# Performance work log

Measured on AMD Instinct MI355X. Metric: run time of the kernel, lower is better.

The kernel has to match this reference:

```python
import jax, jax.numpy as jnp
import numpy as np

B, L, W, MODES, NL, SEG, CM, H1 = 8, 8192, 128, 32, 4, 4, 8, 128


def gelu(x):
    return jax.nn.gelu(x, approximate=False)  # torch nn.GELU default = exact erf


def cft(h, w):
    # h: [b, c, l]; w: [SEG, CM, c_in, c_out] (Chebyshev weights for one layer)
    b, c, l = h.shape
    ls = l // SEG
    xs = h.reshape(b, c, SEG, ls)
    # per-segment global min/max normalization (over batch, channel, position)
    mn = xs.min(axis=(0, 1, 3), keepdims=True)
    mx = xs.max(axis=(0, 1, 3), keepdims=True)
    xn = 2.0 * (xs - mn) / (mx - mn) - 1.0
    Tpp = jnp.ones_like(xn)
    Tp = xn
    coeffs = [(xn * Tpp).mean(-1), (xn * Tp).mean(-1)]  # each [b, c, SEG]
    for _ in range(2, CM):
        Tn = 2.0 * xn * Tp - Tpp
        coeffs.append((xn * Tn).mean(-1))
        Tpp, Tp = Tp, Tn
    C = jnp.stack(coeffs[:CM], axis=-1)  # [b, c, SEG, CM]
    filt = jnp.einsum('bcsm,smco->bcso', C, w)  # per-segment mode filtering
    rec = jnp.tanh(filt.mean(-1))  # [b, c, SEG]
    return jnp.broadcast_to(rec[..., None], (b, c, SEG, ls)).reshape(b, c, l)


def setup_inputs() -> dict:
    key = jax.random.key(0)
    ks = jax.random.split(key, 12)
    scale = 1.0 / (W * W)
    p = {}
    p['x'] = jax.random.normal(ks[0], (B, L, 2), jnp.float32)
    p['fc0_w'] = jax.random.normal(ks[1], (2, W), jnp.float32) * 0.1
    p['fc0_b'] = jnp.zeros((W,), jnp.float32)
    p['spec_wr'] = jax.random.uniform(ks[2], (NL, W, W, MODES), jnp.float32) * scale
    p['spec_wi'] = jax.random.uniform(ks[3], (NL, W, W, MODES), jnp.float32) * scale
    p['conv_w'] = jax.random.normal(ks[4], (NL, W, W), jnp.float32) * 0.05
    p['conv_b'] = jnp.zeros((NL, W), jnp.float32)
    p['cheb_w'] = jax.random.normal(ks[5], (NL, SEG, CM, W, W), jnp.float32) * 0.02
    p['gate_w'] = jax.random.normal(ks[6], (NL, 2 * W, W), jnp.float32) * 0.05
    p['gate_b'] = jnp.zeros((NL, W), jnp.float32)
    p['fc1_w'] = jax.random.normal(ks[7], (W, H1), jnp.float32) * 0.05
    p['fc1_b'] = jnp.zeros((H1,), jnp.float32)
    p['fc2_w'] = jax.random.normal(ks[8], (H1, 1), jnp.float32) * 0.05
    p['fc2_b'] = jnp.zeros((1,), jnp.float32)
    return p


def reference(x, fc0_w, fc0_b, spec_wr, spec_wi, conv_w, conv_b, cheb_w,
              gate_w, gate_b, fc1_w, fc1_b, fc2_w, fc2_b):
    nfreq = L // 2 + 1
    h = x @ fc0_w + fc0_b          # [B, L, W]
    h = h.transpose(0, 2, 1)       # [B, W, L]
    for i in range(NL):
        # --- spectral conv ---
        hf = jnp.fft.rfft(h)       # [B, W, nfreq] complex64
        wgt = spec_wr[i] + 1j * spec_wi[i]
        om = jnp.einsum('bix,iox->box', hf[:, :, :MODES], wgt)
        out_ft = jnp.pad(om, ((0, 0), (0, 0), (0, nfreq - MODES)))
        sp = jnp.fft.irfft(out_ft, n=L)
        # --- 1x1 conv bypass ---
        pw = jnp.einsum('io,bil->bol', conv_w[i], h) + conv_b[i][None, :, None]
        x_fno = gelu(sp + pw)
        # --- CFT branch ---
        x_cft = cft(h, cheb_w[i])
        # --- gated fusion ---
        cat = jnp.concatenate([x_fno, x_cft], axis=1).transpose(0, 2, 1)  # [B, L, 2W]
        gate = jax.nn.sigmoid(cat @ gate_w[i] + gate_b[i]).transpose(0, 2, 1)
        h = x_fno + gate * x_cft
    h = h.transpose(0, 2, 1)       # [B, L, W]
    h = gelu(h @ fc1_w + fc1_b)
    return h @ fc2_w + fc2_b       # [B, L, 1]
```

## Files before the change

### kernel.cpp

```cpp
#include <hip/hip_runtime.h>
#include <math.h>


#define OFF_COSTAB 0
#define OFF_SINTAB 8192
#define OFF_BASTC  16384
#define OFF_BASTS  (OFF_BASTC + 262144)
#define OFF_UNUSED (OFF_BASTS + 262144)
#define OFF_WBAR   (OFF_UNUSED + 65536)
#define OFF_HFP    (OFF_WBAR + 16384)
#define OFF_HF     (OFF_HFP + 1048576)
#define OFF_CH     (OFF_HF + 65536)
#define OFF_REC    (OFF_CH + 32768)
#define OFF_OMCT   (OFF_REC + 4096)
#define OFF_OMST   (OFF_OMCT + 32768)
#define OFF_CG     (OFF_OMST + 32768)
#define OFF_MNMX   (OFF_CG + 4096)
#define OFF_H      (OFF_MNMX + 16)

__device__ __forceinline__ unsigned int enc_f(float f) {
    unsigned int u = __float_as_uint(f);
    return (u & 0x80000000u) ? ~u : (u | 0x80000000u);
}
__device__ __forceinline__ float dec_f(unsigned int u) {
    return (u & 0x80000000u) ? __uint_as_float(u ^ 0x80000000u) : __uint_as_float(~u);
}
__device__ __forceinline__ float gelu_f(float x) {
    return 0.5f * x * (1.0f + erff(x * 0.70710678118654752f));
}
__device__ __forceinline__ float sigmoid_f(float x) {
    return 1.0f / (1.0f + expf(-x));
}

constexpr float C32T[32] = {
    1.0f,          0.980785280f,  0.923879533f,  0.831469612f,
    0.707106781f,  0.555570233f,  0.382683432f,  0.195090322f,
    0.0f,         -0.195090322f, -0.382683432f, -0.555570233f,
   -0.707106781f, -0.831469612f, -0.923879533f, -0.980785280f,
   -1.0f,         -0.980785280f, -0.923879533f, -0.831469612f,
   -0.707106781f, -0.555570233f, -0.382683432f, -0.195090322f,
    0.0f,          0.195090322f,  0.382683432f,  0.555570233f,
    0.707106781f,  0.831469612f,  0.923879533f,  0.980785280f};
constexpr float S32T[32] = {
    0.0f,          0.195090322f,  0.382683432f,  0.555570233f,
    0.707106781f,  0.831469612f,  0.923879533f,  0.980785280f,
    1.0f,          0.980785280f,  0.923879533f,  0.831469612f,
    0.707106781f,  0.555570233f,  0.382683432f,  0.195090322f,
    0.0f,         -0.195090322f, -0.382683432f, -0.555570233f,
   -0.707106781f, -0.831469612f, -0.923879533f, -0.980785280f,
   -1.0f,         -0.980785280f, -0.923879533f, -0.831469612f,
   -0.707106781f, -0.555570233f, -0.382683432f, -0.195090322f};

__global__ void k_tab(float* ws) {
    int m = blockIdx.x * 256 + threadIdx.x;
    if (m < 8192) {
        double a = (double)m * (6.283185307179586476925286766559 / 8192.0);
        ws[OFF_COSTAB + m] = (float)cos(a);
        ws[OFF_SINTAB + m] = (float)sin(a);
    }
}

__global__ void k_init2(float* ws, const float* __restrict__ cheb_w) {
    int tid = blockIdx.x * 256 + threadIdx.x;
    if (tid < 524288) {
        int j = tid >> 13, l = tid & 8191;
        int k = j & 31;
        int tab = (j < 32) ? OFF_COSTAB : OFF_SINTAB;
        ws[OFF_BASTC + tid] = ws[tab + ((k * l) & 8191)];
    } else if (tid < 524288 + 16384) {
        int r = tid - 524288;
        int c = r & 127;
        int smi = r >> 7;
        const float* wp = cheb_w + ((long)smi * 128 + c) * 128;
        float s = 0.0f;
        for (int o = 0; o < 128; o++) s += wp[o];
        ws[OFF_WBAR + r] = s * (1.0f / 128.0f);
    } else if (tid < 524288 + 16384 + 8) {
        int r = tid - (524288 + 16384);
        unsigned int* mm = (unsigned int*)(ws + OFF_MNMX);
        mm[r] = (r < 4) ? 0xFFFFFFFFu : 0u;
    }
}

__global__ __launch_bounds__(256) void k_fc0(float* ws, const float* __restrict__ x,
                                             const float* __restrict__ w,
                                             const float* __restrict__ bias) {
    int bid = blockIdx.x;
    int b = bid >> 5;
    int l0 = (bid & 31) * 256;
    int t = threadIdx.x;
    int l = l0 + t;
    float x0 = x[((long)b * 8192 + l) * 2];
    float x1 = x[((long)b * 8192 + l) * 2 + 1];
    float* hb = ws + OFF_H + (long)b * 128 * 8192;
    float mn = 1e30f, mx = -1e30f;
    for (int c = 0; c < 128; c++) {
        float v = fmaf(x0, w[c], fmaf(x1, w[128 + c], bias[c]));
        hb[(long)c * 8192 + l] = v;
        mn = fminf(mn, v); mx = fmaxf(mx, v);
    }
    for (int off = 32; off; off >>= 1) {
        mn = fminf(mn, __shfl_down(mn, off));
        mx = fmaxf(mx, __shfl_down(mx, off));
    }
    __shared__ float rmn[4], rmx[4];
    if ((t & 63) == 0) { rmn[t >> 6] = mn; rmx[t >> 6] = mx; }
    __syncthreads();
    if (t == 0) {
        for (int w2 = 1; w2 < 4; w2++) { mn = fminf(mn, rmn[w2]); mx = fmaxf(mx, rmx[w2]); }
        unsigned int* mm = (unsigned int*)(ws + OFF_MNMX);
        int seg = l0 >> 11;
        atomicMin(&mm[seg], enc_f(mn));
        atomicMax(&mm[4 + seg], enc_f(mx));
    }
}

__global__ __launch_bounds__(256, 4) void k_dftcb(float* ws, int layer) {
    int row = blockIdx.x;
    int t = threadIdx.x;
    const float* hr = ws + OFF_H + (long)row * 8192;
    __shared__ float red[4][96];
    int wv = t >> 6;

    float ha[32];
    #pragma unroll
    for (int a = 0; a < 32; a++) ha[a] = hr[a * 256 + t];

    const unsigned int* mm = (const unsigned int*)(ws + OFF_MNMX);
    #pragma unroll
    for (int s = 0; s < 4; s++) {
        float mn = dec_f(mm[s]), mx = dec_f(mm[4 + s]);
        float sc = 2.0f / (mx - mn);
        float acc[8] = {};
        #pragma unroll
        for (int e = 0; e < 8; e++) {
            float xn = (ha[s * 8 + e] - mn) * sc - 1.0f;
            float tpp = 1.0f, tp = xn;
            acc[0] += xn;
            acc[1] += xn * xn;
            #pragma unroll
            for (int mI = 2; mI < 8; mI++) {
                float tn = 2.0f * xn * tp - tpp;
                acc[mI] += xn * tn;
                tpp = tp; tp = tn;
            }
        }
        #pragma unroll
        for (int mI = 0; mI < 8; mI++) {
            float v = acc[mI];
            for (int off = 32; off; off >>= 1) v += __shfl_down(v, off);
            if ((t & 63) == 0) red[wv][64 + s * 8 + mI] = v;
        }
    }

    float ep[16], em[16];
    #pragma unroll
    for (int a = 1; a < 16; a++) { ep[a] = ha[a] + ha[32 - a]; em[a] = ha[a] - ha[32 - a]; }
    float h0 = ha[0], h16 = ha[16];
    float Ca[17], Sa[17];
    #pragma unroll
    for (int k = 0; k <= 16; k++) {
        float ca = (k & 1) ? (h0 - h16) : (h0 + h16);
        float sa = 0.0f;
        #pragma unroll
        for (int a = 1; a < 16; a++) {
            ca = fmaf(ep[a], C32T[(k * a) & 31], ca);
            sa = fmaf(em[a], S32T[(k * a) & 31], sa);
        }
        Ca[k] = ca; Sa[k] = sa;
    }

    const float* ct = ws + OFF_COSTAB;
    const float* st = ws + OFF_SINTAB;
    #pragma unroll
    for (int k0 = 0; k0 < 32; k0 += 8) {
        float xr[8], xi[8];
        #pragma unroll
        for (int q = 0; q < 8; q++) {
            int k = k0 + q;
            float caf = (k <= 16) ? Ca[k] : Ca[32 - k];
            float saf = (k <= 16) ? Sa[k] : -Sa[32 - k];
            float c = ct[(k * t) & 8191];
            float s = st[(k * t) & 8191];
            xr[q] = caf * c - saf * s;
            xi[q] = fmaf(saf, c, caf * s);
        }
        #pragma unroll
        for (int q = 0; q < 8; q++) {
            float a = xr[q], b2 = xi[q];
            for (int off = 32; off; off >>= 1) {
                a += __shfl_down(a, off);
                b2 += __shfl_down(b2, off);
            }
            if ((t & 63) == 0) { red[wv][k0 + q] = a; red[wv][32 + k0 + q] = b2; }
        }
    }
    __syncthreads();
    if (t < 96) {
        float s4 = red[0][t] + red[1][t] + red[2][t] + red[3][t];
        if (t < 64) {
            ws[OFF_HF + (long)row * 64 + t] = s4;
        } else {
            red[0][t] = s4 * (1.0f / 2048.0f);
        }
    }
    __syncthreads();
    if (t < 4) {
        const float* wb = ws + OFF_WBAR + ((layer * 4 + t) * 8) * 128 + (row & 127);
        float a = 0.0f;
        #pragma unroll
        for (int mI = 0; mI < 8; mI++) a = fmaf(red[0][64 + t * 8 + mI], wb[mI * 128], a);
        ws[OFF_REC + (long)row * 4 + t] = tanhf(a);
    }
}

__global__ void k_b2(float* ws, const float* __restrict__ swr, const float* __restrict__ swi,
                     const float* __restrict__ gw, const float* __restrict__ gb, int layer) {
    int tid = blockIdx.x * 256 + threadIdx.x;
    if (tid < 32768) {
        int b = tid >> 12, o = (tid >> 5) & 127, k = tid & 31;
        const float* hfb = ws + OFF_HF + (long)b * 8192;
        const float* wr = swr + (long)layer * 524288 + (long)o * 32 + k;
        const float* wi = swi + (long)layer * 524288 + (long)o * 32 + k;
        float omr = 0.0f, omi = 0.0f;
        for (int i = 0; i < 128; i++) {
            float hr = hfb[i * 64 + k];
            float hs = hfb[i * 64 + 32 + k];
            float wrv = wr[(long)i * 4096], wiv = wi[(long)i * 4096];
            omr = fmaf(hr, wrv, fmaf(hs, wiv, omr));
            omi = fmaf(hr, wiv, fmaf(-hs, wrv, omi));
        }
        float ck = (k == 0) ? (1.0f / 8192.0f) : (2.0f / 8192.0f);
        ws[OFF_OMCT + ((long)b * 32 + k) * 128 + o] = ck * omr;
        ws[OFF_OMST + ((long)b * 32 + k) * 128 + o] = -ck * omi;
    } else if (tid < 32768 + 4096) {
        int r = tid - 32768;
        int b = r >> 9, s = (r >> 7) & 3, o = r & 127;
        float a = gb[layer * 128 + o];
        const float* recp = ws + OFF_REC + (long)b * 512 + s;
        const float* g2 = gw + (long)layer * 32768 + 16384 + o;
        for (int c = 0; c < 128; c++) a = fmaf(recp[c * 4], g2[c * 128], a);
        ws[OFF_CG + (long)(b * 4 + s) * 128 + o] = a;
    }
    if (blockIdx.x == gridDim.x - 1 && threadIdx.x < 8) {
        unsigned int* mm = (unsigned int*)(ws + OFF_MNMX);
        mm[threadIdx.x] = (threadIdx.x < 4) ? 0xFFFFFFFFu : 0u;
    }
}

__global__ __launch_bounds__(512, 4) void k_fuse(
    float* __restrict__ hglob,
    const float* __restrict__ basc,
    const float* __restrict__ bass,
    const float* __restrict__ omct,
    const float* __restrict__ omst,
    const float* __restrict__ rec,
    const float* __restrict__ cgt,
    unsigned int* __restrict__ mnmx,
    const float* __restrict__ cw, const float* __restrict__ cb,
    const float* __restrict__ gw, int layer) {
    __shared__ float hx[128 * 128];
    __shared__ float rmn[8], rmx[8];
    int bid = blockIdx.x;
    int b = bid >> 6;
    int l0 = (bid & 63) * 128;
    int seg = l0 >> 11;
    int t = threadIdx.x;
    float* hb = hglob + (long)b * 1048576;

    #pragma unroll
    for (int i = 0; i < 8; i++) {
        int idx = t + i * 512;
        int row = idx >> 5, c4 = (idx & 31) * 4;
        *(float4*)&hx[row * 128 + c4] = *(const float4*)&hb[(long)row * 8192 + l0 + c4];
    }
    __syncthreads();

    int p = t & 63;
    int c0 = __builtin_amdgcn_readfirstlane((t >> 6) * 16);

    float acc0[16] = {}, acc1[16] = {};

    const float* btp = basc + l0 + p;
    const float* bsp = bass + l0 + p;
    const float* omc = omct + (long)b * 4096 + c0;
    const float* oms = omst + (long)b * 4096 + c0;
    #pragma unroll 2
    for (int k = 0; k < 32; k++) {
        float bc0 = btp[k * 8192];
        float bc1 = btp[k * 8192 + 64];
        float bs0 = bsp[k * 8192];
        float bs1 = bsp[k * 8192 + 64];
        #pragma unroll
        for (int c = 0; c < 16; c++) {
            float wc = omc[k * 128 + c], wsn = oms[k * 128 + c];
            acc0[c] = fmaf(wc, bc0, fmaf(wsn, bs0, acc0[c]));
            acc1[c] = fmaf(wc, bc1, fmaf(wsn, bs1, acc1[c]));
        }
    }
    const float* cwt = cw + (long)layer * 16384 + c0;
    #pragma unroll 2
    for (int j = 0; j < 128; j++) {
        float hv0 = hx[j * 128 + p];
        float hv1 = hx[j * 128 + 64 + p];
        #pragma unroll
        for (int c = 0; c < 16; c++) {
            float wv = cwt[j * 128 + c];
            acc0[c] = fmaf(wv, hv0, acc0[c]);
            acc1[c] = fmaf(wv, hv1, acc1[c]);
        }
    }
    const float* cbl = cb + layer * 128 + c0;
    #pragma unroll
    for (int c = 0; c < 16; c++) {
        acc0[c] = gelu_f(acc0[c] + cbl[c]);
        acc1[c] = gelu_f(acc1[c] + cbl[c]);
    }
    __syncthreads();
    #pragma unroll
    for (int c = 0; c < 16; c++) {
        hx[(c0 + c) * 128 + p] = acc0[c];
        hx[(c0 + c) * 128 + 64 + p] = acc1[c];
    }
    __syncthreads();

    const float* gwl = gw + (long)layer * 32768 + c0;
    float gac0[16] = {}, gac1[16] = {};
    #pragma unroll 2
    for (int j = 0; j < 128; j++) {
        float xv0 = hx[j * 128 + p];
        float xv1 = hx[j * 128 + 64 + p];
        #pragma unroll
        for (int c = 0; c < 16; c++) {
            float wv = gwl[j * 128 + c];
            gac0[c] = fmaf(wv, xv0, gac0[c]);
            gac1[c] = fmaf(wv, xv1, gac1[c]);
        }
    }
    const float* cgp = cgt + (long)(b * 4 + seg) * 128 + c0;
    const float* rcp = rec + (long)(b * 128 + c0) * 4 + seg;
    float mnv = 1e30f, mxv = -1e30f;
    #pragma unroll
    for (int c = 0; c < 16; c++) {
        float cgv = cgp[c];
        float rv = rcp[c * 4];
        float g0 = sigmoid_f(gac0[c] + cgv);
        float g1 = sigmoid_f(gac1[c] + cgv);
        float v0 = fmaf(g0, rv, acc0[c]);
        float v1 = fmaf(g1, rv, acc1[c]);
        mnv = fminf(mnv, fminf(v0, v1));
        mxv = fmaxf(mxv, fmaxf(v0, v1));
        hb[(long)(c0 + c) * 8192 + l0 + p] = v0;
        hb[(long)(c0 + c) * 8192 + l0 + 64 + p] = v1;
    }
    for (int off = 32; off; off >>= 1) {
        mnv = fminf(mnv, __shfl_down(mnv, off));
        mxv = fmaxf(mxv, __shfl_down(mxv, off));
    }
    if ((t & 63) == 0) { rmn[t >> 6] = mnv; rmx[t >> 6] = mxv; }
    __syncthreads();
    if (t == 0) {
        for (int w2 = 1; w2 < 8; w2++) { mnv = fminf(mnv, rmn[w2]); mxv = fmaxf(mxv, rmx[w2]); }
        atomicMin(&mnmx[seg], enc_f(mnv));
        atomicMax(&mnmx[4 + seg], enc_f(mxv));
    }
}

__global__ __launch_bounds__(512, 4) void k_fc12(
    const float* __restrict__ hglob, const float* __restrict__ f1w,
    const float* __restrict__ f1b, const float* __restrict__ f2w,
    const float* __restrict__ f2b, float* __restrict__ out) {
    __shared__ float hx[128 * 128];
    int bid = blockIdx.x;
    int b = bid >> 6;
    int l0 = (bid & 63) * 128;
    int t = threadIdx.x;
    const float* hb = hglob + (long)b * 1048576;
    #pragma unroll
    for (int i = 0; i < 8; i++) {
        int idx = t + i * 512;
        int row = idx >> 5, c4 = (idx & 31) * 4;
        *(float4*)&hx[row * 128 + c4] = *(const float4*)&hb[(long)row * 8192 + l0 + c4];
    }
    __syncthreads();
    int p = t & 63;
    int h0 = __builtin_amdgcn_readfirstlane((t >> 6) * 16);
    float acc0[16] = {}, acc1[16] = {};
    const float* f1 = f1w + h0;
    #pragma unroll 2
    for (int j = 0; j < 128; j++) {
        float xv0 = hx[j * 128 + p];
        float xv1 = hx[j * 128 + 64 + p];
        #pragma unroll
        for (int c = 0; c < 16; c++) {
            float wv = f1[j * 128 + c];
            acc0[c] = fmaf(wv, xv0, acc0[c]);
            acc1[c] = fmaf(wv, xv1, acc1[c]);
        }
    }
    float outp0 = 0.0f, outp1 = 0.0f;
    #pragma unroll
    for (int c = 0; c < 16; c++) {
        float bias = f1b[h0 + c];
        float fw = f2w[h0 + c];
        outp0 = fmaf(fw, gelu_f(acc0[c] + bias), outp0);
        outp1 = fmaf(fw, gelu_f(acc1[c] + bias), outp1);
    }
    __syncthreads();
    hx[(t >> 6) * 128 + p] = outp0;
    hx[(t >> 6) * 128 + 64 + p] = outp1;
    __syncthreads();
    if (t < 128) {
        float s = f2b[0];
        #pragma unroll
        for (int gg = 0; gg < 8; gg++) s += hx[gg * 128 + t];
        out[(long)b * 8192 + l0 + t] = s;
    }
}

extern "C" void kernel_launch(void* const* d_in, const int* in_sizes, int n_in,
                              void* d_out, int out_size, void* d_ws, size_t ws_size,
                              hipStream_t stream) {
    const float* x     = (const float*)d_in[0];
    const float* fc0_w = (const float*)d_in[1];
    const float* fc0_b = (const float*)d_in[2];
    const float* swr   = (const float*)d_in[3];
    const float* swi   = (const float*)d_in[4];
    const float* cw    = (const float*)d_in[5];
    const float* cb    = (const float*)d_in[6];
    const float* chw   = (const float*)d_in[7];
    const float* gw    = (const float*)d_in[8];
    const float* gb    = (const float*)d_in[9];
    const float* f1w   = (const float*)d_in[10];
    const float* f1b   = (const float*)d_in[11];
    const float* f2w   = (const float*)d_in[12];
    const float* f2b   = (const float*)d_in[13];
    float* ws = (float*)d_ws;
    float* out = (float*)d_out;

    k_tab<<<32, 256, 0, stream>>>(ws);
    k_init2<<<2112, 256, 0, stream>>>(ws, chw);
    k_fc0<<<256, 256, 0, stream>>>(ws, x, fc0_w, fc0_b);
    for (int layer = 0; layer < 4; layer++) {
        k_dftcb<<<1024, 256, 0, stream>>>(ws, layer);
        k_b2<<<144, 256, 0, stream>>>(ws, swr, swi, gw, gb, layer);
        k_fuse<<<512, 512, 0, stream>>>(ws + OFF_H, ws + OFF_BASTC, ws + OFF_BASTS,
                                        ws + OFF_OMCT, ws + OFF_OMST, ws + OFF_REC,
                                        ws + OFF_CG, (unsigned int*)(ws + OFF_MNMX),
                                        cw, cb, gw, layer);
    }
    k_fc12<<<512, 512, 0, stream>>>(ws + OFF_H, f1w, f1b, f2w, f2b, out);
}
```

Measured before the change: 624.1 us.

## Stage weight matrices through LDS in double-buffered chunks for fuse and fc kernels

Weights for the spectral, pointwise-conv, gate and fc1 matmuls are now loaded cooperatively in 32-row chunks into a 16KB shared buffer, with the next chunk prefetched into registers. Each wave then reads its 16 output weights as broadcast float4 LDS loads. Previously every wave issued uniform scalar global loads per weight. The aim is to cut scalar/global load latency and instruction count in the inner FMA loops. In exchange the kernels use more LDS, which lowers occupancy (80KB per block), and add extra barriers.

```diff
diff --git a/kernel.cpp b/kernel.cpp
--- a/kernel.cpp
+++ b/kernel.cpp
@@ -260,7 +260,7 @@
     const float* __restrict__ cw, const float* __restrict__ cb,
     const float* __restrict__ gw, int layer) {
     __shared__ float hx[128 * 128];
-    __shared__ float rmn[8], rmx[8];
+    __shared__ float wb[4096];
     int bid = blockIdx.x;
     int b = bid >> 6;
     int l0 = (bid & 63) * 128;
@@ -274,69 +274,129 @@
         int row = idx >> 5, c4 = (idx & 31) * 4;
         *(float4*)&hx[row * 128 + c4] = *(const float4*)&hb[(long)row * 8192 + l0 + c4];
     }
-    __syncthreads();
 
     int p = t & 63;
     int c0 = __builtin_amdgcn_readfirstlane((t >> 6) * 16);
+    int srow = t >> 5;
+    int scol = (t & 31) * 4;
 
     float acc0[16] = {}, acc1[16] = {};
 
     const float* btp = basc + l0 + p;
     const float* bsp = bass + l0 + p;
-    const float* omc = omct + (long)b * 4096 + c0;
-    const float* oms = omst + (long)b * 4096 + c0;
-    #pragma unroll 2
-    for (int k = 0; k < 32; k++) {
-        float bc0 = btp[k * 8192];
-        float bc1 = btp[k * 8192 + 64];
-        float bs0 = bsp[k * 8192];
-        float bs1 = bsp[k * 8192 + 64];
-        #pragma unroll
-        for (int c = 0; c < 16; c++) {
-            float wc = omc[k * 128 + c], wsn = oms[k * 128 + c];
-            acc0[c] = fmaf(wc, bc0, fmaf(wsn, bs0, acc0[c]));
-            acc1[c] = fmaf(wc, bc1, fmaf(wsn, bs1, acc1[c]));
-        }
-    }
-    const float* cwt = cw + (long)layer * 16384 + c0;
-    #pragma unroll 2
-    for (int j = 0; j < 128; j++) {
-        float hv0 = hx[j * 128 + p];
-        float hv1 = hx[j * 128 + 64 + p];
-        #pragma unroll
-        for (int c = 0; c < 16; c++) {
-            float wv = cwt[j * 128 + c];
-            acc0[c] = fmaf(wv, hv0, acc0[c]);
-            acc1[c] = fmaf(wv, hv1, acc1[c]);
-        }
-    }
+    const float* omcg = omct + (long)b * 4096;
+    const float* omsg = omst + (long)b * 4096;
+    float4 qa = *(const float4*)&omcg[srow * 128 + scol];
+    float4 qb = *(const float4*)&omsg[srow * 128 + scol];
+    for (int kk = 0; kk < 2; kk++) {
+        __syncthreads();
+        *(float4*)&wb[srow * 128 + scol] = qa;
+        *(float4*)&wb[2048 + srow * 128 + scol] = qb;
+        __syncthreads();
+        if (kk == 0) {
+            qa = *(const float4*)&omcg[2048 + srow * 128 + scol];
+            qb = *(const float4*)&omsg[2048 + srow * 128 + scol];
+        }
+        int kbase = kk * 16;
+        #pragma unroll 4
+        for (int kl = 0; kl < 16; kl++) {
+            int k = kbase + kl;
+            float bc0 = btp[k * 8192];
+            float bc1 = btp[k * 8192 + 64];
+            float bs0 = bsp[k * 8192];
+            float bs1 = bsp[k * 8192 + 64];
+            float wc[16], wsn[16];
+            *(float4*)&wc[0]  = *(const float4*)&wb[kl * 128 + c0];
+            *(float4*)&wc[4]  = *(const float4*)&wb[kl * 128 + c0 + 4];
+            *(float4*)&wc[8]  = *(const float4*)&wb[kl * 128 + c0 + 8];
+            *(float4*)&wc[12] = *(const float4*)&wb[kl * 128 + c0 + 12];
+            *(float4*)&wsn[0]  = *(const float4*)&wb[2048 + kl * 128 + c0];
+            *(float4*)&wsn[4]  = *(const float4*)&wb[2048 + kl * 128 + c0 + 4];
+            *(float4*)&wsn[8]  = *(const float4*)&wb[2048 + kl * 128 + c0 + 8];
+            *(float4*)&wsn[12] = *(const float4*)&wb[2048 + kl * 128 + c0 + 12];
+            #pragma unroll
+            for (int c = 0; c < 16; c++) {
+                acc0[c] = fmaf(wc[c], bc0, fmaf(wsn[c], bs0, acc0[c]));
+                acc1[c] = fmaf(wc[c], bc1, fmaf(wsn[c], bs1, acc1[c]));
+            }
+        }
+    }
+
+    const float* cwt = cw + (long)layer * 16384;
+    qa = *(const float4*)&cwt[srow * 128 + scol];
+    qb = *(const float4*)&cwt[2048 + srow * 128 + scol];
+    for (int jc = 0; jc < 4; jc++) {
+        __syncthreads();
+        *(float4*)&wb[srow * 128 + scol] = qa;
+        *(float4*)&wb[2048 + srow * 128 + scol] = qb;
+        __syncthreads();
+        if (jc < 3) {
+            qa = *(const float4*)&cwt[(jc + 1) * 4096 + srow * 128 + scol];
+            qb = *(const float4*)&cwt[(jc + 1) * 4096 + 2048 + srow * 128 + scol];
+        }
+        int jbase = jc * 32;
+        #pragma unroll 4
+        for (int jl = 0; jl < 32; jl++) {
+            float hv0 = hx[(jbase + jl) * 128 + p];
+            float hv1 = hx[(jbase + jl) * 128 + 64 + p];
+            float wv[16];
+            *(float4*)&wv[0]  = *(const float4*)&wb[jl * 128 + c0];
+            *(float4*)&wv[4]  = *(const float4*)&wb[jl * 128 + c0 + 4];
+            *(float4*)&wv[8]  = *(const float4*)&wb[jl * 128 + c0 + 8];
+            *(float4*)&wv[12] = *(const float4*)&wb[jl * 128 + c0 + 12];
+            #pragma unroll
+            for (int c = 0; c < 16; c++) {
+                acc0[c] = fmaf(wv[c], hv0, acc0[c]);
+                acc1[c] = fmaf(wv[c], hv1, acc1[c]);
+            }
+        }
+    }
+
+    const float* gwt = gw + (long)layer * 32768;
+    qa = *(const float4*)&gwt[srow * 128 + scol];
+    qb = *(const float4*)&gwt[2048 + srow * 128 + scol];
     const float* cbl = cb + layer * 128 + c0;
+    float xf0[16], xf1[16];
     #pragma unroll
     for (int c = 0; c < 16; c++) {
-        acc0[c] = gelu_f(acc0[c] + cbl[c]);
-        acc1[c] = gelu_f(acc1[c] + cbl[c]);
+        xf0[c] = gelu_f(acc0[c] + cbl[c]);
+        xf1[c] = gelu_f(acc1[c] + cbl[c]);
     }
     __syncthreads();
     #pragma unroll
     for (int c = 0; c < 16; c++) {
-        hx[(c0 + c) * 128 + p] = acc0[c];
-        hx[(c0 + c) * 128 + 64 + p] = acc1[c];
-    }
-    __syncthreads();
-
-    const float* gwl = gw + (long)layer * 32768 + c0;
+        hx[(c0 + c) * 128 + p] = xf0[c];
+        hx[(c0 + c) * 128 + 64 + p] = xf1[c];
+    }
+
     float gac0[16] = {}, gac1[16] = {};
-    #pragma unroll 2
-    for (int j = 0; j < 128; j++) {
-        float xv0 = hx[j * 128 + p];
-        float xv1 = hx[j * 128 + 64 + p];
-        #pragma unroll
-        for (int c = 0; c < 16; c++) {
-            float wv = gwl[j * 128 + c];
-            gac0[c] = fmaf(wv, xv0, gac0[c]);
-            gac1[c] = fmaf(wv, xv1, gac1[c]);
-        }
-    }
+    for (int jc = 0; jc < 4; jc++) {
+        __syncthreads();
+        *(float4*)&wb[srow * 128 + scol] = qa;
+        *(float4*)&wb[2048 + srow * 128 + scol] = qb;
+        __syncthreads();
+        if (jc < 3) {
+            qa = *(const float4*)&gwt[(jc + 1) * 4096 + srow * 128 + scol];
+            qb = *(const float4*)&gwt[(jc + 1) * 4096 + 2048 + srow * 128 + scol];
+        }
+        int jbase = jc * 32;
+        #pragma unroll 4
+        for (int jl = 0; jl < 32; jl++) {
+            float xv0 = hx[(jbase + jl) * 128 + p];
+            float xv1 = hx[(jbase + jl) * 128 + 64 + p];
+            float wv[16];
+            *(float4*)&wv[0]  = *(const float4*)&wb[jl * 128 + c0];
+            *(float4*)&wv[4]  = *(const float4*)&wb[jl * 128 + c0 + 4];
+            *(float4*)&wv[8]  = *(const float4*)&wb[jl * 128 + c0 + 8];
+            *(float4*)&wv[12] = *(const float4*)&wb[jl * 128 + c0 + 12];
+            #pragma unroll
+            for (int c = 0; c < 16; c++) {
+                gac0[c] = fmaf(wv[c], xv0, gac0[c]);
+                gac1[c] = fmaf(wv[c], xv1, gac1[c]);
+            }
+        }
+    }
+
     const float* cgp = cgt + (long)(b * 4 + seg) * 128 + c0;
     const float* rcp = rec + (long)(b * 128 + c0) * 4 + seg;
     float mnv = 1e30f, mxv = -1e30f;
@@ -346,8 +406,8 @@
         float rv = rcp[c * 4];
         float g0 = sigmoid_f(gac0[c] + cgv);
         float g1 = sigmoid_f(gac1[c] + cgv);
-        float v0 = fmaf(g0, rv, acc0[c]);
-        float v1 = fmaf(g1, rv, acc1[c]);
+        float v0 = fmaf(g0, rv, xf0[c]);
+        float v1 = fmaf(g1, rv, xf1[c]);
         mnv = fminf(mnv, fminf(v0, v1));
         mxv = fmaxf(mxv, fmaxf(v0, v1));
         hb[(long)(c0 + c) * 8192 + l0 + p] = v0;
@@ -357,10 +417,11 @@
         mnv = fminf(mnv, __shfl_down(mnv, off));
         mxv = fmaxf(mxv, __shfl_down(mxv, off));
     }
-    if ((t & 63) == 0) { rmn[t >> 6] = mnv; rmx[t >> 6] = mxv; }
+    __syncthreads();
+    if ((t & 63) == 0) { wb[t >> 6] = mnv; wb[8 + (t >> 6)] = mxv; }
     __syncthreads();
     if (t == 0) {
-        for (int w2 = 1; w2 < 8; w2++) { mnv = fminf(mnv, rmn[w2]); mxv = fmaxf(mxv, rmx[w2]); }
+        for (int w2 = 1; w2 < 8; w2++) { mnv = fminf(mnv, wb[w2]); mxv = fmaxf(mxv, wb[8 + w2]); }
         atomicMin(&mnmx[seg], enc_f(mnv));
         atomicMax(&mnmx[4 + seg], enc_f(mxv));
     }
@@ -371,6 +432,7 @@
     const float* __restrict__ f1b, const float* __restrict__ f2w,
     const float* __restrict__ f2b, float* __restrict__ out) {
     __shared__ float hx[128 * 128];
+    __shared__ float wb[4096];
     int bid = blockIdx.x;
     int b = bid >> 6;
     int l0 = (bid & 63) * 128;
@@ -382,20 +444,37 @@
         int row = idx >> 5, c4 = (idx & 31) * 4;
         *(float4*)&hx[row * 128 + c4] = *(const float4*)&hb[(long)row * 8192 + l0 + c4];
     }
-    __syncthreads();
     int p = t & 63;
     int h0 = __builtin_amdgcn_readfirstlane((t >> 6) * 16);
+    int srow = t >> 5;
+    int scol = (t & 31) * 4;
     float acc0[16] = {}, acc1[16] = {};
-    const float* f1 = f1w + h0;
-    #pragma unroll 2
-    for (int j = 0; j < 128; j++) {
-        float xv0 = hx[j * 128 + p];
-        float xv1 = hx[j * 128 + 64 + p];
-        #pragma unroll
-        for (int c = 0; c < 16; c++) {
-            float wv = f1[j * 128 + c];
-            acc0[c] = fmaf(wv, xv0, acc0[c]);
-            acc1[c] = fmaf(wv, xv1, acc1[c]);
+    float4 qa = *(const float4*)&f1w[srow * 128 + scol];
+    float4 qb = *(const float4*)&f1w[2048 + srow * 128 + scol];
+    for (int jc = 0; jc < 4; jc++) {
+        __syncthreads();
+        *(float4*)&wb[srow * 128 + scol] = qa;
+        *(float4*)&wb[2048 + srow * 128 + scol] = qb;
+        __syncthreads();
+        if (jc < 3) {
+            qa = *(const float4*)&f1w[(jc + 1) * 4096 + srow * 128 + scol];
+            qb = *(const float4*)&f1w[(jc + 1) * 4096 + 2048 + srow * 128 + scol];
+        }
+        int jbase = jc * 32;
+        #pragma unroll 4
+        for (int jl = 0; jl < 32; jl++) {
+            float xv0 = hx[(jbase + jl) * 128 + p];
+            float xv1 = hx[(jbase + jl) * 128 + 64 + p];
+            float wv[16];
+            *(float4*)&wv[0]  = *(const float4*)&wb[jl * 128 + h0];
+            *(float4*)&wv[4]  = *(const float4*)&wb[jl * 128 + h0 + 4];
+            *(float4*)&wv[8]  = *(const float4*)&wb[jl * 128 + h0 + 8];
+            *(float4*)&wv[12] = *(const float4*)&wb[jl * 128 + h0 + 12];
+            #pragma unroll
+            for (int c = 0; c < 16; c++) {
+                acc0[c] = fmaf(wv[c], xv0, acc0[c]);
+                acc1[c] = fmaf(wv[c], xv1, acc1[c]);
+            }
         }
     }
     float outp0 = 0.0f, outp1 = 0.0f;
```

After: 706.5 us. 1.13x slower.
